# Performance work log

Hardware: AMD Instinct MI355X
Metric: run time of the kernel (lower is better)

Reference implementation:

```python
import jax, jax.numpy as jnp
import numpy as np

SLOT_SIZE = 64
START_IDX = 0  # slot2idx['<start>']
STOP_IDX = 1   # slot2idx['<stop>']
NEG_INF = -10000.0


def setup_inputs() -> dict:
    key = jax.random.key(0)
    k1, k2 = jax.random.split(key)
    B, T, S = 512, 512, SLOT_SIZE
    logits = jax.random.normal(k1, (B, T, S), dtype=jnp.float32)
    masks = jnp.ones((B, T), dtype=jnp.float32)
    # nn.Parameter(torch.randn(S, S)) with START/STOP constraints from __init__
    transitions = jax.random.normal(k2, (S, S), dtype=jnp.float32)
    transitions = transitions.at[START_IDX, :].set(NEG_INF)
    transitions = transitions.at[:, STOP_IDX].set(NEG_INF)
    return {"logits": logits, "masks": masks, "transitions": transitions}


def reference(logits, masks, transitions):
    """Faithful CRF.forward == _viterbi_decode(logits, masks).

    Replicates the original quirks:
      - masks multiply only the emission feat (transitions are NOT masked
        inside the Viterbi recursion);
      - path_score is taken from the LAST next_tag's (next_tag = S-1)
        score vector at the final timestep, and the backtrace is seeded
        from that same column's argmax;
      - the backtrace re-applies the last backpointer table once before
        walking backwards (exactly as the torch loop does), and the
        popped start tag is dropped, giving a (B, T-1) path.
    """
    B, T, S = logits.shape
    init = jnp.full((B, S), NEG_INF, dtype=logits.dtype).at[:, START_IDX].set(0.0)

    # masked emissions for timesteps 1..T-1, time-major for scan: (T-1, B, S)
    feats = jnp.swapaxes(logits[:, 1:, :] * masks[:, 1:, None], 0, 1)

    def step(fv, feat_t):
        # scores[b, next, prev] = fv[b, prev] + transitions[next, prev]
        scores = fv[:, None, :] + transitions[None, :, :]  # (B, S, S)
        bptr = jnp.argmax(scores, axis=2).astype(jnp.int32)  # (B, S)
        vmax = jnp.max(scores, axis=2)                       # (B, S)
        return vmax + feat_t, (bptr, vmax)

    _, (bptrs, vmaxs) = jax.lax.scan(step, init, feats)  # (T-1, B, S) each

    # torch quirk: next_tag_var / best_tag_id left over from next_tag = S-1
    path_score = vmaxs[-1][:, S - 1]          # (B,)
    t0 = bptrs[-1][:, S - 1]                  # (B,) seed for backtrace

    def back(tag, bp):
        new_tag = jnp.take_along_axis(bp, tag[:, None], axis=1)[:, 0]
        return new_tag, tag  # emit the tag BEFORE following the pointer

    # reverse scan walks bptrs from last to first; emitted ys land at their
    # original time index, so ys == reversed best_path (start tag dropped
    # because the final carry -- the start tag -- is never emitted).
    _, ys = jax.lax.scan(back, t0, bptrs, reverse=True)  # (T-1, B)
    best_seq = jnp.swapaxes(ys, 0, 1)  # (B, T-1)
    return path_score, best_seq
```

## Files before the change

kernel.cpp:

```cpp
#include <hip/hip_runtime.h>


constexpr int Bz = 512;
constexpr int Tz = 512;
constexpr int Sz = 64;
constexpr float NEGINF = -10000.0f;

__global__ __launch_bounds__(512)
void crf_viterbi_kernel(const float* __restrict__ logits,
                        const float* __restrict__ masks,
                        const float* __restrict__ trans,
                        float* __restrict__ out)
{
    const int n = threadIdx.x & 63;
    const int w = threadIdx.x >> 6;
    const int b = blockIdx.x;

    __shared__ unsigned bp[128 * 64];
    __shared__ int2 pvi[8][64];
    __shared__ float fvs[64];
    __shared__ float ys[Tz - 1];

    float tr[8];
    {
        const float4* tr4 = reinterpret_cast<const float4*>(trans + n * 64 + 8 * w);
        float4 t0 = tr4[0], t1 = tr4[1];
        tr[0] = t0.x; tr[1] = t0.y; tr[2] = t0.z; tr[3] = t0.w;
        tr[4] = t1.x; tr[5] = t1.y; tr[6] = t1.z; tr[7] = t1.w;
    }

    if (threadIdx.x < 64) fvs[n] = (n == 0) ? 0.0f : NEGINF;

    const float* lgbase = logits + (size_t)b * Tz * Sz;
    const float* mkbase = masks + (size_t)b * Tz;

    float lg0 = lgbase[1 * Sz + n];
    float lg1 = lgbase[2 * Sz + n];
    unsigned pk = 0;
    float psc = 0.0f;

    __syncthreads();

    #pragma unroll 4
    for (int i = 0; i < Tz - 1; ++i) {
        const float4* fv4 = reinterpret_cast<const float4*>(&fvs[8 * w]);
        float4 f0 = fv4[0], f1 = fv4[1];

        float v[8];
        v[0] = f0.x + tr[0]; v[1] = f0.y + tr[1];
        v[2] = f0.z + tr[2]; v[3] = f0.w + tr[3];
        v[4] = f1.x + tr[4]; v[5] = f1.y + tr[5];
        v[6] = f1.z + tr[6]; v[7] = f1.w + tr[7];

        float m01 = fmaxf(v[0], v[1]), m23 = fmaxf(v[2], v[3]);
        float m45 = fmaxf(v[4], v[5]), m67 = fmaxf(v[6], v[7]);
        float lm  = fmaxf(fmaxf(m01, m23), fmaxf(m45, m67));

        int li = 7;
        #pragma unroll
        for (int j = 6; j >= 0; --j) li = (v[j] == lm) ? j : li;

        pvi[w][n] = make_int2(__float_as_int(lm), li);
        __syncthreads();

        const int grp = i >> 2;
        if (w == (grp & 7)) {
            float cv[8]; int ci[8];
            #pragma unroll
            for (int q = 0; q < 8; ++q) {
                int2 p = pvi[q][n];
                cv[q] = __int_as_float(p.x);
                ci[q] = 8 * q + p.y;
            }
            float a01 = fmaxf(cv[0], cv[1]), a23 = fmaxf(cv[2], cv[3]);
            float a45 = fmaxf(cv[4], cv[5]), a67 = fmaxf(cv[6], cv[7]);
            float m   = fmaxf(fmaxf(a01, a23), fmaxf(a45, a67));

            int gi = ci[7];
            #pragma unroll
            for (int q = 6; q >= 0; --q) gi = (cv[q] == m) ? ci[q] : gi;

            if (i == Tz - 2) psc = m;

            pk |= ((unsigned)gi) << (8 * (i & 3));
            if ((i & 3) == 3) { bp[grp * 64 + n] = pk; pk = 0; }

            float mk = mkbase[i + 1];
            fvs[n] = m + lg0 * mk;
        }
        __syncthreads();

        lg0 = lg1;
        int t3 = (i + 3 < Tz) ? (i + 3) : (Tz - 1);
        lg1 = lgbase[t3 * Sz + n];
    }

    if (w == 7) {
        bp[127 * 64 + n] = pk;
        if (n == 63) out[b] = psc;
    }

    __syncthreads();

    if (w == 0) {
        unsigned wcur = bp[127 * 64 + n];
        int w127_63 = __builtin_amdgcn_readlane((int)wcur, 63);
        int tag = (w127_63 >> 16) & 255;

        for (int g = 127; g >= 0; --g) {
            unsigned wnext = (g > 0) ? bp[(g - 1) * 64 + n] : 0u;
            int smax = (g == 127) ? 2 : 3;
            for (int s = smax; s >= 0; --s) {
                int idx = 4 * g + s;
                if (n == 0) ys[idx] = (float)tag;
                int wd = __builtin_amdgcn_readlane((int)wcur, tag);
                tag = (wd >> (8 * s)) & 255;
            }
            wcur = wnext;
        }
    }

    __syncthreads();

    float* outseq = out + Bz + (size_t)b * (Tz - 1);
    for (int k = threadIdx.x; k < Tz - 1; k += 512) outseq[k] = ys[k];
}

extern "C" void kernel_launch(void* const* d_in, const int* in_sizes, int n_in,
                              void* d_out, int out_size, void* d_ws, size_t ws_size,
                              hipStream_t stream) {
    const float* logits = (const float*)d_in[0];
    const float* masks  = (const float*)d_in[1];
    const float* trans  = (const float*)d_in[2];
    float* out = (float*)d_out;
    (void)in_sizes; (void)n_in; (void)out_size; (void)d_ws; (void)ws_size;

    crf_viterbi_kernel<<<dim3(Bz), dim3(512), 0, stream>>>(logits, masks, trans, out);
}
```

Baseline: 352.8 us.

## Replicate the Viterbi combine in every wave and broadcast scores via readlane

Every wave now redundantly performs the cross-wave max/argmax reduction and keeps the forward vector in a register. Previous-state scores are broadcast with readlane instead of being read from shared memory. The partial-result buffer is double-buffered, so one barrier per timestep replaces two. Logits and masks are prefetched four steps ahead. The cost is duplicated reduction work in all eight waves and extra scalar readlane instructions.

```diff
diff --git a/kernel.cpp b/kernel.cpp
--- a/kernel.cpp
+++ b/kernel.cpp
@@ -5,6 +5,10 @@
 constexpr int Tz = 512;
 constexpr int Sz = 64;
 constexpr float NEGINF = -10000.0f;
+
+__device__ __forceinline__ float rlf(float x, int lane) {
+    return __int_as_float(__builtin_amdgcn_readlane(__float_as_int(x), lane));
+}
 
 __global__ __launch_bounds__(512)
 void crf_viterbi_kernel(const float* __restrict__ logits,
@@ -15,91 +19,93 @@
     const int n = threadIdx.x & 63;
     const int w = threadIdx.x >> 6;
     const int b = blockIdx.x;
+    const int pb = 8 * w;
 
     __shared__ unsigned bp[128 * 64];
-    __shared__ int2 pvi[8][64];
-    __shared__ float fvs[64];
+    __shared__ int2 pvi[2][8][64];
     __shared__ float ys[Tz - 1];
 
     float tr[8];
     {
-        const float4* tr4 = reinterpret_cast<const float4*>(trans + n * 64 + 8 * w);
+        const float4* tr4 = reinterpret_cast<const float4*>(trans + n * 64 + pb);
         float4 t0 = tr4[0], t1 = tr4[1];
         tr[0] = t0.x; tr[1] = t0.y; tr[2] = t0.z; tr[3] = t0.w;
         tr[4] = t1.x; tr[5] = t1.y; tr[6] = t1.z; tr[7] = t1.w;
     }
 
-    if (threadIdx.x < 64) fvs[n] = (n == 0) ? 0.0f : NEGINF;
+    float fv = (n == 0) ? 0.0f : NEGINF;
 
     const float* lgbase = logits + (size_t)b * Tz * Sz;
     const float* mkbase = masks + (size_t)b * Tz;
 
-    float lg0 = lgbase[1 * Sz + n];
-    float lg1 = lgbase[2 * Sz + n];
+    float lg0 = lgbase[1 * Sz + n], lg1 = lgbase[2 * Sz + n];
+    float lg2 = lgbase[3 * Sz + n], lg3 = lgbase[4 * Sz + n];
+    float mk0 = mkbase[1], mk1 = mkbase[2], mk2 = mkbase[3], mk3 = mkbase[4];
+
     unsigned pk = 0;
     float psc = 0.0f;
 
-    __syncthreads();
-
     #pragma unroll 4
     for (int i = 0; i < Tz - 1; ++i) {
-        const float4* fv4 = reinterpret_cast<const float4*>(&fvs[8 * w]);
-        float4 f0 = fv4[0], f1 = fv4[1];
+        float v0 = rlf(fv, pb + 0) + tr[0];
+        float v1 = rlf(fv, pb + 1) + tr[1];
+        float v2 = rlf(fv, pb + 2) + tr[2];
+        float v3 = rlf(fv, pb + 3) + tr[3];
+        float v4 = rlf(fv, pb + 4) + tr[4];
+        float v5 = rlf(fv, pb + 5) + tr[5];
+        float v6 = rlf(fv, pb + 6) + tr[6];
+        float v7 = rlf(fv, pb + 7) + tr[7];
 
-        float v[8];
-        v[0] = f0.x + tr[0]; v[1] = f0.y + tr[1];
-        v[2] = f0.z + tr[2]; v[3] = f0.w + tr[3];
-        v[4] = f1.x + tr[4]; v[5] = f1.y + tr[5];
-        v[6] = f1.z + tr[6]; v[7] = f1.w + tr[7];
+        float m01 = fmaxf(v0, v1), m23 = fmaxf(v2, v3);
+        float m45 = fmaxf(v4, v5), m67 = fmaxf(v6, v7);
+        float lm  = fmaxf(fmaxf(m01, m23), fmaxf(m45, m67));
+        int li = 7;
+        li = (v6 == lm) ? 6 : li;
+        li = (v5 == lm) ? 5 : li;
+        li = (v4 == lm) ? 4 : li;
+        li = (v3 == lm) ? 3 : li;
+        li = (v2 == lm) ? 2 : li;
+        li = (v1 == lm) ? 1 : li;
+        li = (v0 == lm) ? 0 : li;
 
-        float m01 = fmaxf(v[0], v[1]), m23 = fmaxf(v[2], v[3]);
-        float m45 = fmaxf(v[4], v[5]), m67 = fmaxf(v[6], v[7]);
-        float lm  = fmaxf(fmaxf(m01, m23), fmaxf(m45, m67));
-
-        int li = 7;
-        #pragma unroll
-        for (int j = 6; j >= 0; --j) li = (v[j] == lm) ? j : li;
-
-        pvi[w][n] = make_int2(__float_as_int(lm), li);
+        pvi[i & 1][w][n] = make_int2(__float_as_int(lm), pb + li);
         __syncthreads();
 
-        const int grp = i >> 2;
-        if (w == (grp & 7)) {
-            float cv[8]; int ci[8];
-            #pragma unroll
-            for (int q = 0; q < 8; ++q) {
-                int2 p = pvi[q][n];
-                cv[q] = __int_as_float(p.x);
-                ci[q] = 8 * q + p.y;
-            }
-            float a01 = fmaxf(cv[0], cv[1]), a23 = fmaxf(cv[2], cv[3]);
-            float a45 = fmaxf(cv[4], cv[5]), a67 = fmaxf(cv[6], cv[7]);
-            float m   = fmaxf(fmaxf(a01, a23), fmaxf(a45, a67));
+        float cv[8]; int ci[8];
+        #pragma unroll
+        for (int q = 0; q < 8; ++q) {
+            int2 p = pvi[i & 1][q][n];
+            cv[q] = __int_as_float(p.x);
+            ci[q] = p.y;
+        }
+        float a01 = fmaxf(cv[0], cv[1]), a23 = fmaxf(cv[2], cv[3]);
+        float a45 = fmaxf(cv[4], cv[5]), a67 = fmaxf(cv[6], cv[7]);
+        float m   = fmaxf(fmaxf(a01, a23), fmaxf(a45, a67));
+        int gi = ci[7];
+        #pragma unroll
+        for (int q = 6; q >= 0; --q) gi = (cv[q] == m) ? ci[q] : gi;
 
-            int gi = ci[7];
-            #pragma unroll
-            for (int q = 6; q >= 0; --q) gi = (cv[q] == m) ? ci[q] : gi;
+        if (i == Tz - 2) psc = m;
 
-            if (i == Tz - 2) psc = m;
+        pk |= ((unsigned)gi) << (8 * (i & 3));
+        if ((i & 3) == 3) {
+            if (w == ((i >> 2) & 7)) bp[(i >> 2) * 64 + n] = pk;
+            pk = 0;
+        }
 
-            pk |= ((unsigned)gi) << (8 * (i & 3));
-            if ((i & 3) == 3) { bp[grp * 64 + n] = pk; pk = 0; }
+        fv = m + lg0 * mk0;
 
-            float mk = mkbase[i + 1];
-            fvs[n] = m + lg0 * mk;
-        }
-        __syncthreads();
-
-        lg0 = lg1;
-        int t3 = (i + 3 < Tz) ? (i + 3) : (Tz - 1);
-        lg1 = lgbase[t3 * Sz + n];
+        lg0 = lg1; lg1 = lg2; lg2 = lg3;
+        mk0 = mk1; mk1 = mk2; mk2 = mk3;
+        int tnext = (i + 5 < Tz) ? (i + 5) : (Tz - 1);
+        lg3 = lgbase[tnext * Sz + n];
+        mk3 = mkbase[tnext];
     }
 
     if (w == 7) {
         bp[127 * 64 + n] = pk;
         if (n == 63) out[b] = psc;
     }
-
     __syncthreads();
 
     if (w == 0) {
@@ -119,7 +125,6 @@
             wcur = wnext;
         }
     }
-
     __syncthreads();
 
     float* outseq = out + Bz + (size_t)b * (Tz - 1);
```

Result: slower. 424.1 us (+20.2%).
